# Performance work log

Measured on AMD Instinct MI355X. Metric: run time of the kernel, lower is better.

## Reference

```python
import jax, jax.numpy as jnp
import numpy as np

BETA = 0.25  # commitment loss weight


def setup_inputs() -> dict:
    key = jax.random.key(0)
    k1, k2 = jax.random.split(key)
    N, K, d = 131072, 1024, 64
    z_e = jax.random.normal(k1, (N, d), dtype=jnp.float32)
    scale = 1.0 / np.sqrt(d)
    codebook = jax.random.uniform(k2, (K, d), minval=-scale, maxval=scale, dtype=jnp.float32)
    return {"z_e": z_e, "codebook": codebook}


def reference(z_e, codebook):
    d = codebook.shape[-1]
    flat = z_e.reshape(-1, d)                                  # (N, d)
    z_sq = jnp.sum(flat ** 2, axis=-1, keepdims=True)          # (N, 1)
    c_sq = jnp.sum(codebook ** 2, axis=-1)[None, :]            # (1, K)
    zc = flat @ codebook.T                                     # (N, K)
    dists = z_sq - 2.0 * zc + c_sq
    idx_flat = jnp.argmin(dists, axis=-1)                      # (N,)
    e_flat = codebook[idx_flat]                                # (N, d)
    z_q_flat_st = flat + jax.lax.stop_gradient(e_flat - flat)  # straight-through
    codebook_loss = jnp.mean((e_flat - jax.lax.stop_gradient(flat)) ** 2)
    commitment_loss = jnp.mean((jax.lax.stop_gradient(e_flat) - flat) ** 2)
    vq_loss = codebook_loss + BETA * commitment_loss
    indices = idx_flat.reshape(z_e.shape[:-1])
    z_q_st = z_q_flat_st.reshape(z_e.shape)
    return (indices, z_q_st, vq_loss)
```

## Files before the change

### kernel.cpp

```cpp
#include <hip/hip_runtime.h>
#include <stdint.h>

#define DIM 64
#define KC 1024
#define TAU_HALF 5.0e-4f
#define FLAG_CAP 16384

typedef float f32x4 __attribute__((ext_vector_type(4)));
typedef short short8 __attribute__((ext_vector_type(8)));

__device__ __forceinline__ unsigned short bf16_rn(float f) {
  union { float f; uint32_t u; } v; v.f = f;
  uint32_t u = v.u;
  uint32_t r = u + 0x7fffu + ((u >> 16) & 1u);
  return (unsigned short)(r >> 16);
}
__device__ __forceinline__ float bf16_f32(unsigned short h) {
  union { uint32_t u; float f; } v; v.u = ((uint32_t)h) << 16;
  return v.f;
}

__global__ void k1_prep(const float* __restrict__ cb,
                        unsigned short* __restrict__ cb_hi,
                        unsigned short* __restrict__ cb_lo,
                        float* __restrict__ csqh,
                        int* __restrict__ cnt) {
  const int k = blockIdx.x, j = threadIdx.x;
  const float c = cb[k * DIM + j];
  const unsigned short hi = bf16_rn(c);
  const float hif = bf16_f32(hi);
  const unsigned short lo = bf16_rn(c - hif);
  cb_hi[k * DIM + j] = hi;
  cb_lo[k * DIM + j] = lo;
  float s = c * c;
  #pragma unroll
  for (int off = 32; off >= 1; off >>= 1) s += __shfl_xor(s, off);
  if (j == 0) csqh[k] = -0.5f * s;
  if (k == 0 && j == 0) *cnt = 0;
}

__launch_bounds__(256, 2)
__global__ void k2_argmin(const float* __restrict__ z,
                          const unsigned short* __restrict__ cb_hi,
                          const unsigned short* __restrict__ cb_lo,
                          const float* __restrict__ csqh,
                          float* __restrict__ out_idx,
                          int* __restrict__ cnt,
                          int* __restrict__ flags) {
  __shared__ unsigned short lds_cb[2 * 128 * 64];
  __shared__ float lds_csq[KC];
  __shared__ float lds_m1[2][128];
  __shared__ float lds_m2[2][128];
  __shared__ int   lds_i1[2][128];

  const int tid  = threadIdx.x;
  const int lane = tid & 63;
  const int wv   = tid >> 6;
  const int wr   = wv >> 1;
  const int wc   = wv & 1;
  const int lg   = lane >> 4;
  const int lr   = lane & 15;
  const int row0 = blockIdx.x * 128;

  ((f32x4*)lds_csq)[tid] = ((const f32x4*)csqh)[tid];

  short8 zhi[4][2], zlo[4][2];
  #pragma unroll
  for (int rt = 0; rt < 4; ++rt) {
    const int row = row0 + wr * 64 + rt * 16 + lr;
    #pragma unroll
    for (int ks = 0; ks < 2; ++ks) {
      const float* p = z + row * DIM + ks * 32 + lg * 8;
      const f32x4 va = *(const f32x4*)p;
      const f32x4 vb = *(const f32x4*)(p + 4);
      union { uint32_t w[4]; short8 s8; } H, L;
      #pragma unroll
      for (int pr = 0; pr < 4; ++pr) {
        const float f0 = (pr < 2) ? va[2 * pr]     : vb[2 * pr - 4];
        const float f1 = (pr < 2) ? va[2 * pr + 1] : vb[2 * pr - 3];
        const uint32_t u0 = __float_as_uint(f0);
        const uint32_t u1 = __float_as_uint(f1);
        H.w[pr] = __builtin_amdgcn_perm(u1, u0, 0x07060302u);
        const float l0 = f0 - __uint_as_float(u0 & 0xffff0000u);
        const float l1 = f1 - __uint_as_float(u1 & 0xffff0000u);
        uint32_t lw;
        asm("v_cvt_pk_bf16_f32 %0, %1, %2" : "=v"(lw) : "v"(l0), "v"(l1));
        L.w[pr] = lw;
      }
      zhi[rt][ks] = H.s8;
      zlo[rt][ks] = L.s8;
    }
  }

  float M1[4], M2[4];
  int I1[4];
  #pragma unroll
  for (int rt = 0; rt < 4; ++rt) { M1[rt] = -3.0e38f; M2[rt] = -3.0e38f; I1[rt] = 0; }

  for (int t = 0; t < KC / 128; ++t) {
    __syncthreads();
    #pragma unroll
    for (int p = 0; p < 8; ++p) {
      const int linear = p * 256 + tid;
      const int chunk  = linear & 7;
      const int cl     = (linear >> 3) & 127;
      const int split  = linear >> 10;
      const unsigned short* src = (split ? cb_lo : cb_hi) + (t * 128 + cl) * DIM + chunk * 8;
      const uint4 v = *(const uint4*)src;
      const int dst = split * 16384 + cl * 128 + ((chunk * 16) ^ ((cl & 7) << 4));
      *(uint4*)((char*)lds_cb + dst) = v;
    }
    __syncthreads();

    const int iterbase = t * 128 + wc * 64;
    #pragma unroll
    for (int ct = 0; ct < 4; ++ct) {
      const int cbase = iterbase + ct * 16 + lg * 4;
      const f32x4 init = *(const f32x4*)&lds_csq[cbase];
      short8 cfrag[2][2];
      #pragma unroll
      for (int sp = 0; sp < 2; ++sp) {
        #pragma unroll
        for (int ks = 0; ks < 2; ++ks) {
          const int cl2 = wc * 64 + ct * 16 + lr;
          const int chunk = ks * 4 + lg;
          const int off = sp * 16384 + cl2 * 128 + ((chunk * 16) ^ ((cl2 & 7) << 4));
          cfrag[sp][ks] = *(const short8*)((const char*)lds_cb + off);
        }
      }
      #pragma unroll
      for (int rt = 0; rt < 4; ++rt) {
        f32x4 acc = init;
        acc = __builtin_amdgcn_mfma_f32_16x16x32_bf16(cfrag[0][0], zhi[rt][0], acc, 0, 0, 0);
        acc = __builtin_amdgcn_mfma_f32_16x16x32_bf16(cfrag[0][1], zhi[rt][1], acc, 0, 0, 0);
        acc = __builtin_amdgcn_mfma_f32_16x16x32_bf16(cfrag[0][0], zlo[rt][0], acc, 0, 0, 0);
        acc = __builtin_amdgcn_mfma_f32_16x16x32_bf16(cfrag[0][1], zlo[rt][1], acc, 0, 0, 0);
        acc = __builtin_amdgcn_mfma_f32_16x16x32_bf16(cfrag[1][0], zhi[rt][0], acc, 0, 0, 0);
        acc = __builtin_amdgcn_mfma_f32_16x16x32_bf16(cfrag[1][1], zhi[rt][1], acc, 0, 0, 0);
        #pragma unroll
        for (int j = 0; j < 4; ++j) {
          const float s = acc[j];
          M2[rt] = __builtin_amdgcn_fmed3f(s, M1[rt], M2[rt]);
          const bool take = s > M1[rt];
          M1[rt] = fmaxf(s, M1[rt]);
          I1[rt] = take ? (cbase + j) : I1[rt];
        }
      }
    }
  }

  #pragma unroll
  for (int rt = 0; rt < 4; ++rt) {
    float m1 = M1[rt], m2 = M2[rt];
    int i1 = I1[rt];
    #pragma unroll
    for (int off = 16; off <= 32; off <<= 1) {
      const float o1 = __shfl_xor(m1, off);
      const float o2 = __shfl_xor(m2, off);
      const int   oi = __shfl_xor(i1, off);
      m2 = fmaxf(fmaxf(m2, o2), fminf(m1, o1));
      const bool take = (o1 > m1) || (o1 == m1 && oi < i1);
      if (take) { m1 = o1; i1 = oi; }
    }
    if (lg == 0) {
      const int r = wr * 64 + rt * 16 + lr;
      lds_m1[wc][r] = m1;
      lds_m2[wc][r] = m2;
      lds_i1[wc][r] = i1;
    }
  }
  __syncthreads();
  if (tid < 128) {
    const float a1 = lds_m1[0][tid], b1 = lds_m1[1][tid];
    const float a2 = lds_m2[0][tid], b2 = lds_m2[1][tid];
    const int   ai = lds_i1[0][tid], bi = lds_i1[1][tid];
    const bool takeB = (b1 > a1) || (b1 == a1 && bi < ai);
    const float m1 = takeB ? b1 : a1;
    const int  idx = takeB ? bi : ai;
    const float m2 = fmaxf(fmaxf(a2, b2), fminf(a1, b1));
    const int row = row0 + tid;
    out_idx[row] = (float)idx;
    if (m1 - m2 < TAU_HALF) {
      const int p = atomicAdd(cnt, 1);
      if (p < FLAG_CAP) flags[p] = row;
    }
  }
}

__global__ void k3_rescue(const float* __restrict__ z,
                          const float* __restrict__ cb,
                          const float* __restrict__ csqh,
                          float* __restrict__ out_idx,
                          const int* __restrict__ cnt,
                          const int* __restrict__ flags) {
  __shared__ float zrow[DIM];
  __shared__ float rv[256];
  __shared__ int   ri[256];
  const int tid = threadIdx.x;
  int n = *cnt;
  if (n > FLAG_CAP) n = FLAG_CAP;
  for (int i = blockIdx.x; i < n; i += gridDim.x) {
    const int row = flags[i];
    __syncthreads();
    if (tid < DIM) zrow[tid] = z[row * DIM + tid];
    __syncthreads();
    float m1 = -3.0e38f;
    int i1 = 0;
    for (int k = tid; k < KC; k += 256) {
      const f32x4* cp = (const f32x4*)(cb + k * DIM);
      float acc = csqh[k];
      #pragma unroll
      for (int j4 = 0; j4 < DIM / 4; ++j4) {
        const f32x4 c4 = cp[j4];
        acc = fmaf(zrow[j4 * 4 + 0], c4[0], acc);
        acc = fmaf(zrow[j4 * 4 + 1], c4[1], acc);
        acc = fmaf(zrow[j4 * 4 + 2], c4[2], acc);
        acc = fmaf(zrow[j4 * 4 + 3], c4[3], acc);
      }
      if (acc > m1) { m1 = acc; i1 = k; }
    }
    rv[tid] = m1; ri[tid] = i1;
    __syncthreads();
    for (int s = 128; s >= 1; s >>= 1) {
      if (tid < s) {
        const float o = rv[tid + s];
        const int  oi = ri[tid + s];
        if (o > rv[tid] || (o == rv[tid] && oi < ri[tid])) { rv[tid] = o; ri[tid] = oi; }
      }
      __syncthreads();
    }
    if (tid == 0) out_idx[row] = (float)ri[0];
    __syncthreads();
  }
}

__global__ void k4_finalize(const float* __restrict__ z,
                            const float* __restrict__ cb,
                            const float* __restrict__ out_idx,
                            float* __restrict__ zq,
                            float* __restrict__ partials) {
  __shared__ float wsum[4];
  const int tid = threadIdx.x;
  const int rl = tid >> 4;
  const int q  = tid & 15;
  const int row = blockIdx.x * 16 + rl;
  const int idx = (int)out_idx[row];
  const f32x4 e  = ((const f32x4*)cb)[idx * 16 + q];
  const f32x4 zz = ((const f32x4*)z)[row * 16 + q];
  ((f32x4*)zq)[row * 16 + q] = e;
  const float d0 = e[0] - zz[0], d1 = e[1] - zz[1], d2 = e[2] - zz[2], d3 = e[3] - zz[3];
  float partial = d0 * d0 + d1 * d1 + d2 * d2 + d3 * d3;
  #pragma unroll
  for (int off = 32; off >= 1; off >>= 1) partial += __shfl_xor(partial, off);
  if ((tid & 63) == 0) wsum[tid >> 6] = partial;
  __syncthreads();
  if (tid == 0) partials[blockIdx.x] = wsum[0] + wsum[1] + wsum[2] + wsum[3];
}

__global__ void k5_reduce(const float* __restrict__ partials,
                          float* __restrict__ loss_slot,
                          float scale, int nb) {
  __shared__ float wsum[4];
  const int tid = threadIdx.x;
  float s = 0.0f;
  for (int i = tid; i < nb / 4; i += 256) {
    const f32x4 v = ((const f32x4*)partials)[i];
    s += (v[0] + v[1]) + (v[2] + v[3]);
  }
  #pragma unroll
  for (int off = 32; off >= 1; off >>= 1) s += __shfl_xor(s, off);
  if ((tid & 63) == 0) wsum[tid >> 6] = s;
  __syncthreads();
  if (tid == 0) *loss_slot = (wsum[0] + wsum[1] + wsum[2] + wsum[3]) * scale;
}

extern "C" void kernel_launch(void* const* d_in, const int* in_sizes, int n_in,
                              void* d_out, int out_size, void* d_ws, size_t ws_size,
                              hipStream_t stream) {
  const float* z  = (const float*)d_in[0];
  const float* cb = (const float*)d_in[1];
  const int N = in_sizes[0] / DIM;

  float* out       = (float*)d_out;
  float* out_idx   = out;
  float* zq        = out + N;
  float* loss_slot = out + N + (size_t)N * DIM;

  unsigned short* cb_hi = (unsigned short*)d_ws;
  unsigned short* cb_lo = cb_hi + KC * DIM;
  float* csqh = (float*)(cb_lo + KC * DIM);
  int* cnt    = (int*)(csqh + KC);
  int* flags  = cnt + 64;
  float* partials = (float*)(flags + FLAG_CAP);

  const int nb4 = N / 16;
  const float scale = 1.25f / ((float)N * (float)DIM);

  k1_prep<<<KC, DIM, 0, stream>>>(cb, cb_hi, cb_lo, csqh, cnt);
  k2_argmin<<<N / 128, 256, 0, stream>>>(z, cb_hi, cb_lo, csqh, out_idx, cnt, flags);
  k3_rescue<<<128, 256, 0, stream>>>(z, cb, csqh, out_idx, cnt, flags);
  k4_finalize<<<nb4, 256, 0, stream>>>(z, cb, out_idx, zq, partials);
  k5_reduce<<<1, 256, 0, stream>>>(partials, loss_slot, scale, nb4);
}
```

Baseline: 188.7 us.

## Pipeline codebook tiles via async LDS loads and fuse loss into argmin kernel

The argmin kernel now double-buffers 64-code codebook tiles with global_load_lds, using one barrier per tile, and raises the occupancy target to 4 blocks per CU. The loss is computed inside argmin from |z|^2 - 2*max score, so the finalize kernel no longer reads z and becomes a plain codebook gather. The rescue kernel assigns one wavefront per flagged row with a shuffle reduction instead of a whole block with LDS reductions. The goals are to hide codebook load latency, drop a full pass over z, and cut synchronisation. The fused loss uses bf16-split scores, so it may differ slightly from the exact loss, and rows fixed by the rescue kernel still carry the loss term of their pre-rescue code.

```diff
diff --git a/kernel.cpp b/kernel.cpp
--- a/kernel.cpp
+++ b/kernel.cpp
@@ -3,6 +3,8 @@
 
 #define DIM 64
 #define KC 1024
+#define TILE 64
+#define NT (KC / TILE)
 #define TAU_HALF 5.0e-4f
 #define FLAG_CAP 16384
 
@@ -18,6 +20,11 @@
 __device__ __forceinline__ float bf16_f32(unsigned short h) {
   union { uint32_t u; float f; } v; v.u = ((uint32_t)h) << 16;
   return v.f;
+}
+__device__ __forceinline__ void gll16(const void* g, void* l) {
+  __builtin_amdgcn_global_load_lds(
+      (const __attribute__((address_space(1))) void*)g,
+      (__attribute__((address_space(3))) void*)l, 16, 0, 0);
 }
 
 __global__ void k1_prep(const float* __restrict__ cb,
@@ -39,19 +46,17 @@
   if (k == 0 && j == 0) *cnt = 0;
 }
 
-__launch_bounds__(256, 2)
+__launch_bounds__(256, 4)
 __global__ void k2_argmin(const float* __restrict__ z,
                           const unsigned short* __restrict__ cb_hi,
                           const unsigned short* __restrict__ cb_lo,
                           const float* __restrict__ csqh,
                           float* __restrict__ out_idx,
                           int* __restrict__ cnt,
-                          int* __restrict__ flags) {
-  __shared__ unsigned short lds_cb[2 * 128 * 64];
+                          int* __restrict__ flags,
+                          float* __restrict__ partials) {
+  __shared__ unsigned short lds_cb[2 * 8192];
   __shared__ float lds_csq[KC];
-  __shared__ float lds_m1[2][128];
-  __shared__ float lds_m2[2][128];
-  __shared__ int   lds_i1[2][128];
 
   const int tid  = threadIdx.x;
   const int lane = tid & 63;
@@ -62,17 +67,42 @@
   const int lr   = lane & 15;
   const int row0 = blockIdx.x * 128;
 
+  const unsigned short* gsrc[4];
+  #pragma unroll
+  for (int p = 0; p < 4; ++p) {
+    const int cl = (p & 1) * 32 + wv * 8 + (lane >> 3);
+    const int ch = (lane & 7) ^ (cl & 7);
+    gsrc[p] = ((p >> 1) ? cb_lo : cb_hi) + cl * DIM + ch * 8;
+  }
+
+#define STAGE(tt, bs)                                                         \
+  {                                                                           \
+    const int _toff = (tt) * (TILE * DIM);                                    \
+    _Pragma("unroll")                                                         \
+    for (int p = 0; p < 4; ++p) {                                             \
+      gll16(gsrc[p] + _toff,                                                  \
+            (char*)lds_cb + (bs) * 16384 + (p * 256 + wv * 64) * 16);         \
+    }                                                                         \
+  }
+
+  STAGE(0, 0);
   ((f32x4*)lds_csq)[tid] = ((const f32x4*)csqh)[tid];
 
   short8 zhi[4][2], zlo[4][2];
+  float zsq[4];
   #pragma unroll
   for (int rt = 0; rt < 4; ++rt) {
     const int row = row0 + wr * 64 + rt * 16 + lr;
+    float sq = 0.0f;
     #pragma unroll
     for (int ks = 0; ks < 2; ++ks) {
       const float* p = z + row * DIM + ks * 32 + lg * 8;
       const f32x4 va = *(const f32x4*)p;
       const f32x4 vb = *(const f32x4*)(p + 4);
+      sq = fmaf(va[0], va[0], sq); sq = fmaf(va[1], va[1], sq);
+      sq = fmaf(va[2], va[2], sq); sq = fmaf(va[3], va[3], sq);
+      sq = fmaf(vb[0], vb[0], sq); sq = fmaf(vb[1], vb[1], sq);
+      sq = fmaf(vb[2], vb[2], sq); sq = fmaf(vb[3], vb[3], sq);
       union { uint32_t w[4]; short8 s8; } H, L;
       #pragma unroll
       for (int pr = 0; pr < 4; ++pr) {
@@ -90,6 +120,7 @@
       zhi[rt][ks] = H.s8;
       zlo[rt][ks] = L.s8;
     }
+    zsq[rt] = sq;
   }
 
   float M1[4], M2[4];
@@ -97,46 +128,34 @@
   #pragma unroll
   for (int rt = 0; rt < 4; ++rt) { M1[rt] = -3.0e38f; M2[rt] = -3.0e38f; I1[rt] = 0; }
 
-  for (int t = 0; t < KC / 128; ++t) {
-    __syncthreads();
-    #pragma unroll
-    for (int p = 0; p < 8; ++p) {
-      const int linear = p * 256 + tid;
-      const int chunk  = linear & 7;
-      const int cl     = (linear >> 3) & 127;
-      const int split  = linear >> 10;
-      const unsigned short* src = (split ? cb_lo : cb_hi) + (t * 128 + cl) * DIM + chunk * 8;
-      const uint4 v = *(const uint4*)src;
-      const int dst = split * 16384 + cl * 128 + ((chunk * 16) ^ ((cl & 7) << 4));
-      *(uint4*)((char*)lds_cb + dst) = v;
-    }
-    __syncthreads();
-
-    const int iterbase = t * 128 + wc * 64;
-    #pragma unroll
-    for (int ct = 0; ct < 4; ++ct) {
-      const int cbase = iterbase + ct * 16 + lg * 4;
+  __syncthreads();
+
+  for (int t = 0; t < NT; ++t) {
+    if (t < NT - 1) STAGE(t + 1, (t + 1) & 1);
+    const char* bufb = (const char*)lds_cb + (t & 1) * 16384;
+    #pragma unroll
+    for (int ct = 0; ct < 2; ++ct) {
+      const int cbase = t * TILE + wc * 32 + ct * 16 + lg * 4;
       const f32x4 init = *(const f32x4*)&lds_csq[cbase];
-      short8 cfrag[2][2];
+      const int cl2 = wc * 32 + ct * 16 + lr;
+      short8 cf[2][2];
       #pragma unroll
       for (int sp = 0; sp < 2; ++sp) {
         #pragma unroll
         for (int ks = 0; ks < 2; ++ks) {
-          const int cl2 = wc * 64 + ct * 16 + lr;
-          const int chunk = ks * 4 + lg;
-          const int off = sp * 16384 + cl2 * 128 + ((chunk * 16) ^ ((cl2 & 7) << 4));
-          cfrag[sp][ks] = *(const short8*)((const char*)lds_cb + off);
+          const int off = sp * 8192 + cl2 * 128 + (((ks * 4 + lg) ^ (cl2 & 7)) * 16);
+          cf[sp][ks] = *(const short8*)(bufb + off);
         }
       }
       #pragma unroll
       for (int rt = 0; rt < 4; ++rt) {
         f32x4 acc = init;
-        acc = __builtin_amdgcn_mfma_f32_16x16x32_bf16(cfrag[0][0], zhi[rt][0], acc, 0, 0, 0);
-        acc = __builtin_amdgcn_mfma_f32_16x16x32_bf16(cfrag[0][1], zhi[rt][1], acc, 0, 0, 0);
-        acc = __builtin_amdgcn_mfma_f32_16x16x32_bf16(cfrag[0][0], zlo[rt][0], acc, 0, 0, 0);
-        acc = __builtin_amdgcn_mfma_f32_16x16x32_bf16(cfrag[0][1], zlo[rt][1], acc, 0, 0, 0);
-        acc = __builtin_amdgcn_mfma_f32_16x16x32_bf16(cfrag[1][0], zhi[rt][0], acc, 0, 0, 0);
-        acc = __builtin_amdgcn_mfma_f32_16x16x32_bf16(cfrag[1][1], zhi[rt][1], acc, 0, 0, 0);
+        acc = __builtin_amdgcn_mfma_f32_16x16x32_bf16(cf[0][0], zhi[rt][0], acc, 0, 0, 0);
+        acc = __builtin_amdgcn_mfma_f32_16x16x32_bf16(cf[0][1], zhi[rt][1], acc, 0, 0, 0);
+        acc = __builtin_amdgcn_mfma_f32_16x16x32_bf16(cf[0][0], zlo[rt][0], acc, 0, 0, 0);
+        acc = __builtin_amdgcn_mfma_f32_16x16x32_bf16(cf[0][1], zlo[rt][1], acc, 0, 0, 0);
+        acc = __builtin_amdgcn_mfma_f32_16x16x32_bf16(cf[1][0], zhi[rt][0], acc, 0, 0, 0);
+        acc = __builtin_amdgcn_mfma_f32_16x16x32_bf16(cf[1][1], zhi[rt][1], acc, 0, 0, 0);
         #pragma unroll
         for (int j = 0; j < 4; ++j) {
           const float s = acc[j];
@@ -147,7 +166,14 @@
         }
       }
     }
-  }
+    __syncthreads();
+  }
+
+  float* S  = (float*)lds_cb;
+  float* S2 = S + 256;
+  int*   SI = (int*)(S + 512);
+  float* ZS = (float*)(SI + 256);
+  float* CT = ZS + 128;
 
   #pragma unroll
   for (int rt = 0; rt < 4; ++rt) {
@@ -162,29 +188,42 @@
       const bool take = (o1 > m1) || (o1 == m1 && oi < i1);
       if (take) { m1 = o1; i1 = oi; }
     }
+    float zq = zsq[rt];
+    zq += __shfl_xor(zq, 16);
+    zq += __shfl_xor(zq, 32);
     if (lg == 0) {
       const int r = wr * 64 + rt * 16 + lr;
-      lds_m1[wc][r] = m1;
-      lds_m2[wc][r] = m2;
-      lds_i1[wc][r] = i1;
+      S[wc * 128 + r]  = m1;
+      S2[wc * 128 + r] = m2;
+      SI[wc * 128 + r] = i1;
+      if (wc == 0) ZS[r] = zq;
     }
   }
   __syncthreads();
   if (tid < 128) {
-    const float a1 = lds_m1[0][tid], b1 = lds_m1[1][tid];
-    const float a2 = lds_m2[0][tid], b2 = lds_m2[1][tid];
-    const int   ai = lds_i1[0][tid], bi = lds_i1[1][tid];
+    const float a1 = S[tid],  b1 = S[128 + tid];
+    const float a2 = S2[tid], b2 = S2[128 + tid];
+    const int   ai = SI[tid], bi = SI[128 + tid];
     const bool takeB = (b1 > a1) || (b1 == a1 && bi < ai);
     const float m1 = takeB ? b1 : a1;
     const int  idx = takeB ? bi : ai;
     const float m2 = fmaxf(fmaxf(a2, b2), fminf(a1, b1));
     const int row = row0 + tid;
     out_idx[row] = (float)idx;
+    CT[tid] = ZS[tid] - 2.0f * m1;
     if (m1 - m2 < TAU_HALF) {
       const int p = atomicAdd(cnt, 1);
       if (p < FLAG_CAP) flags[p] = row;
     }
   }
+  __syncthreads();
+  if (tid < 64) {
+    float c = CT[tid] + CT[tid + 64];
+    #pragma unroll
+    for (int off = 32; off >= 1; off >>= 1) c += __shfl_xor(c, off);
+    if (tid == 0) partials[blockIdx.x] = c;
+  }
+#undef STAGE
 }
 
 __global__ void k3_rescue(const float* __restrict__ z,
@@ -193,68 +232,50 @@
                           float* __restrict__ out_idx,
                           const int* __restrict__ cnt,
                           const int* __restrict__ flags) {
-  __shared__ float zrow[DIM];
-  __shared__ float rv[256];
-  __shared__ int   ri[256];
-  const int tid = threadIdx.x;
   int n = *cnt;
   if (n > FLAG_CAP) n = FLAG_CAP;
-  for (int i = blockIdx.x; i < n; i += gridDim.x) {
+  const int lane = threadIdx.x & 63;
+  const int w = blockIdx.x * 4 + (threadIdx.x >> 6);
+  for (int i = w; i < n; i += gridDim.x * 4) {
     const int row = flags[i];
-    __syncthreads();
-    if (tid < DIM) zrow[tid] = z[row * DIM + tid];
-    __syncthreads();
+    const f32x4* zr4 = (const f32x4*)(z + (size_t)row * DIM);
     float m1 = -3.0e38f;
     int i1 = 0;
-    for (int k = tid; k < KC; k += 256) {
-      const f32x4* cp = (const f32x4*)(cb + k * DIM);
+    for (int kk = 0; kk < 16; ++kk) {
+      const int k = lane * 16 + kk;
+      const f32x4* cp = (const f32x4*)(cb + (size_t)k * DIM);
       float acc = csqh[k];
       #pragma unroll
       for (int j4 = 0; j4 < DIM / 4; ++j4) {
         const f32x4 c4 = cp[j4];
-        acc = fmaf(zrow[j4 * 4 + 0], c4[0], acc);
-        acc = fmaf(zrow[j4 * 4 + 1], c4[1], acc);
-        acc = fmaf(zrow[j4 * 4 + 2], c4[2], acc);
-        acc = fmaf(zrow[j4 * 4 + 3], c4[3], acc);
+        const f32x4 z4 = zr4[j4];
+        acc = fmaf(z4[0], c4[0], acc);
+        acc = fmaf(z4[1], c4[1], acc);
+        acc = fmaf(z4[2], c4[2], acc);
+        acc = fmaf(z4[3], c4[3], acc);
       }
       if (acc > m1) { m1 = acc; i1 = k; }
     }
-    rv[tid] = m1; ri[tid] = i1;
-    __syncthreads();
-    for (int s = 128; s >= 1; s >>= 1) {
-      if (tid < s) {
-        const float o = rv[tid + s];
-        const int  oi = ri[tid + s];
-        if (o > rv[tid] || (o == rv[tid] && oi < ri[tid])) { rv[tid] = o; ri[tid] = oi; }
-      }
-      __syncthreads();
-    }
-    if (tid == 0) out_idx[row] = (float)ri[0];
-    __syncthreads();
-  }
-}
-
-__global__ void k4_finalize(const float* __restrict__ z,
-                            const float* __restrict__ cb,
-                            const float* __restrict__ out_idx,
-                            float* __restrict__ zq,
-                            float* __restrict__ partials) {
-  __shared__ float wsum[4];
-  const int tid = threadIdx.x;
-  const int rl = tid >> 4;
-  const int q  = tid & 15;
-  const int row = blockIdx.x * 16 + rl;
+    #pragma unroll
+    for (int off = 32; off >= 1; off >>= 1) {
+      const float o1 = __shfl_xor(m1, off);
+      const int   oi = __shfl_xor(i1, off);
+      if (o1 > m1 || (o1 == m1 && oi < i1)) { m1 = o1; i1 = oi; }
+    }
+    if (lane == 0) out_idx[row] = (float)i1;
+  }
+}
+
+__global__ void k4_scatter(const float* __restrict__ cb,
+                           const float* __restrict__ out_idx,
+                           float* __restrict__ zq) {
+  const int gid = blockIdx.x * 256 + threadIdx.x;
+  const int row = gid >> 2;
+  const int q0  = (gid & 3) * 4;
   const int idx = (int)out_idx[row];
-  const f32x4 e  = ((const f32x4*)cb)[idx * 16 + q];
-  const f32x4 zz = ((const f32x4*)z)[row * 16 + q];
-  ((f32x4*)zq)[row * 16 + q] = e;
-  const float d0 = e[0] - zz[0], d1 = e[1] - zz[1], d2 = e[2] - zz[2], d3 = e[3] - zz[3];
-  float partial = d0 * d0 + d1 * d1 + d2 * d2 + d3 * d3;
-  #pragma unroll
-  for (int off = 32; off >= 1; off >>= 1) partial += __shfl_xor(partial, off);
-  if ((tid & 63) == 0) wsum[tid >> 6] = partial;
-  __syncthreads();
-  if (tid == 0) partials[blockIdx.x] = wsum[0] + wsum[1] + wsum[2] + wsum[3];
+  const f32x4* src = (const f32x4*)(cb + (size_t)idx * DIM) + q0;
+  f32x4* dst = (f32x4*)(zq + (size_t)row * DIM) + q0;
+  dst[0] = src[0]; dst[1] = src[1]; dst[2] = src[2]; dst[3] = src[3];
 }
 
 __global__ void k5_reduce(const float* __restrict__ partials,
@@ -293,12 +314,12 @@
   int* flags  = cnt + 64;
   float* partials = (float*)(flags + FLAG_CAP);
 
-  const int nb4 = N / 16;
+  const int nb2 = N / 128;
   const float scale = 1.25f / ((float)N * (float)DIM);
 
   k1_prep<<<KC, DIM, 0, stream>>>(cb, cb_hi, cb_lo, csqh, cnt);
-  k2_argmin<<<N / 128, 256, 0, stream>>>(z, cb_hi, cb_lo, csqh, out_idx, cnt, flags);
-  k3_rescue<<<128, 256, 0, stream>>>(z, cb, csqh, out_idx, cnt, flags);
-  k4_finalize<<<nb4, 256, 0, stream>>>(z, cb, out_idx, zq, partials);
-  k5_reduce<<<1, 256, 0, stream>>>(partials, loss_slot, scale, nb4);
-}
+  k2_argmin<<<nb2, 256, 0, stream>>>(z, cb_hi, cb_lo, csqh, out_idx, cnt, flags, partials);
+  k3_rescue<<<256, 256, 0, stream>>>(z, cb, csqh, out_idx, cnt, flags);
+  k4_scatter<<<N / 64, 256, 0, stream>>>(cb, out_idx, zq);
+  k5_reduce<<<1, 256, 0, stream>>>(partials, loss_slot, scale, nb2);
+}
```

New measurement: 185.5 us. About the same (-1.7%).
